# Kernel tuning notes

Measured on AMD Instinct MI355X. Metric: run time of the kernel, lower is better.

Reference implementation:

```python
import jax, jax.numpy as jnp
import numpy as np
import math

B, NB, NA, NC, D, E, H = 4, 2048, 1024, 1024, 1024, 8, 16
HD = D // H
TOP_K = 2
T_MAX = 1000.0
TAU_MIN, TAU_MAX = 0.5, 2.0
W_MIN, W_MAX = 0.1, 0.2
CAP_LO, CAP_HI = 0.5, 0.6
FLOOR = min(0.05, 0.15 / E)       # cfg.routing_floor property
ALPHA = min(FLOOR * E, 1.0)       # routing-floor interpolation weight
BIAS_COEFF = 0.01
EPS = 1e-8


def _layernorm(x, g, b, eps=1e-5):
    mu = x.mean(-1, keepdims=True)
    var = ((x - mu) ** 2).mean(-1, keepdims=True)
    return (x - mu) * jax.lax.rsqrt(var + eps) * g + b


def _forward(tokens_B, output_A, output_C, in_proj_w, in_proj_b, out_proj_w, out_proj_b,
             ln_g, ln_b, te_w1, te_b1, te_w2, te_b2,
             gate_w1, gate_b1, gate_w2, gate_b2, expert_bias, t):
    t_norm = t.astype(jnp.float32) / T_MAX                 # (B,)
    ctx_C = jax.lax.stop_gradient(output_C)                # stopgrad_C_to_B
    ctx_AC = jnp.concatenate([output_A, ctx_C], axis=1)    # (B, NA+NC, D)

    # --- cross attention (torch nn.MultiheadAttention, batch_first) ---
    wq, wk, wv = jnp.split(in_proj_w, 3, axis=0)
    bq, bk, bv = jnp.split(in_proj_b, 3)
    q = (tokens_B @ wq.T + bq).reshape(B, NB, H, HD)
    k = (ctx_AC @ wk.T + bk).reshape(B, NA + NC, H, HD)
    v = (ctx_AC @ wv.T + bv).reshape(B, NA + NC, H, HD)
    scores = jnp.einsum('bqhd,bkhd->bhqk', q, k) / math.sqrt(HD)
    attn = jax.nn.softmax(scores, axis=-1)
    ctx = jnp.einsum('bhqk,bkhd->bqhd', attn, v).reshape(B, NB, D)
    ctx_B = ctx @ out_proj_w.T + out_proj_b
    ctx_B = _layernorm(ctx_B + tokens_B, ln_g, ln_b)

    # --- sinusoidal timestep embedding + 2-layer MLP ---
    half = D // 2
    freq = jnp.exp(-math.log(10000.0) * jnp.arange(half, dtype=jnp.float32) / (half - 1))
    args = t.astype(jnp.float32)[:, None] * freq
    emb = jnp.concatenate([jnp.sin(args), jnp.cos(args)], axis=-1)   # (B, D)
    t_emb = jax.nn.silu(emb @ te_w1.T + te_b1) @ te_w2.T + te_b2     # (B, D)
    t_emb = jnp.broadcast_to(t_emb[:, None, :], (B, NB, D))

    # --- gate MLP + expert bias + temperature ---
    gate_in = jnp.concatenate([tokens_B, ctx_B, t_emb], axis=-1)     # (B, NB, 3D)
    logits = jax.nn.relu(gate_in @ gate_w1.T + gate_b1) @ gate_w2.T + gate_b2 + expert_bias
    tau = (TAU_MIN + (TAU_MAX - TAU_MIN) * t_norm)[:, None, None]
    probs = jax.nn.softmax(logits / tau, axis=-1)                    # (B, NB, E)

    # routing floor: interpolate toward uniform
    probs = (1.0 - ALPHA) * probs + ALPHA / E

    # shared expert injection: expert 0 gets scheduled weight w(t), rest renormalised
    w = (W_MIN + (W_MAX - W_MIN) * t_norm)[:, None, None]
    shared = jnp.maximum(probs[..., 0:1], w)
    others = probs[..., 1:]
    others = others / jnp.maximum(others.sum(-1, keepdims=True), EPS) * (1.0 - shared)
    probs = jnp.concatenate([shared, others], axis=-1)

    # top-k mask (keep top-k probs, zero the rest)
    vals, idx = jax.lax.top_k(probs, TOP_K)
    dispatch = (jax.nn.one_hot(idx, E, dtype=probs.dtype) * vals[..., None]).sum(-2)

    # token-level hard cap (torch.no_grad -> stop_gradient) with redistribution
    cap = (CAP_LO + (CAP_HI - CAP_LO) * t_norm)[:, None, None]
    excess = jax.nn.relu(dispatch - cap)
    capped = dispatch - excess
    headroom = jax.nn.relu(cap - capped)
    head_sum = jnp.maximum(headroom.sum(-1, keepdims=True), EPS)
    capped = capped + excess.sum(-1, keepdims=True) * (headroom / head_sum)
    dispatch = jax.lax.stop_gradient(capped)

    # batch-level utilisation penalty on specialists 1..E-1
    fair = NB / max(E - 1, 1)
    load = dispatch.sum(axis=1).mean(axis=0)                          # (E,)
    pen_excess = jax.nn.relu(load[1:] - fair * 1.5)
    bias_penalty = BIAS_COEFF * jnp.sum(pen_excess ** 2)

    combine = dispatch / (dispatch.sum(-1, keepdims=True) + EPS)
    return dispatch, combine, bias_penalty


def setup_inputs() -> dict:
    key = jax.random.key(0)
    ks = jax.random.split(key, 12)
    g = lambda k, sh: jax.random.normal(k, sh, jnp.float32) * 0.02
    return dict(
        tokens_B=jax.random.normal(ks[0], (B, NB, D), jnp.float32),
        output_A=jax.random.normal(ks[1], (B, NA, D), jnp.float32),
        output_C=jax.random.normal(ks[2], (B, NC, D), jnp.float32),
        t=jax.random.randint(ks[3], (B,), 0, 1000, jnp.int32),
        in_proj_w=g(ks[4], (3 * D, D)),
        in_proj_b=jnp.zeros((3 * D,), jnp.float32),
        out_proj_w=g(ks[5], (D, D)),
        out_proj_b=jnp.zeros((D,), jnp.float32),
        ln_g=jnp.ones((D,), jnp.float32),
        ln_b=jnp.zeros((D,), jnp.float32),
        te_w1=g(ks[6], (2 * D, D)),
        te_b1=jnp.zeros((2 * D,), jnp.float32),
        te_w2=g(ks[7], (D, 2 * D)),
        te_b2=jnp.zeros((D,), jnp.float32),
        gate_w1=g(ks[8], (D, 3 * D)),
        gate_b1=jnp.zeros((D,), jnp.float32),
        gate_w2=g(ks[9], (E, D)),
        gate_b2=jnp.zeros((E,), jnp.float32),
        expert_bias=jnp.zeros((E,), jnp.float32),
    )


def reference(tokens_B, output_A, output_C, t, in_proj_w, in_proj_b, out_proj_w, out_proj_b,
              ln_g, ln_b, te_w1, te_b1, te_w2, te_b2,
              gate_w1, gate_b1, gate_w2, gate_b2, expert_bias):
    return _forward(tokens_B, output_A, output_C, in_proj_w, in_proj_b, out_proj_w, out_proj_b,
                    ln_g, ln_b, te_w1, te_b1, te_w2, te_b2,
                    gate_w1, gate_b1, gate_w2, gate_b2, expert_bias, t)
```

## Files before the change

kernel.cpp:

```cpp
#include <hip/hip_runtime.h>
#include <math.h>


typedef __attribute__((ext_vector_type(8))) short short8;
typedef __attribute__((ext_vector_type(4))) short sh4;
typedef __attribute__((ext_vector_type(4))) float f32x4;
typedef __attribute__((ext_vector_type(4))) unsigned int u32x4;
typedef unsigned short u16;
typedef unsigned int u32;

__global__ void zero_k(double* p) {
    if (threadIdx.x < 8) p[threadIdx.x] = 0.0;
}

__device__ inline u16 bf_hi(float x) {
    u32 u = __float_as_uint(x);
    u += 0x7FFFu + ((u >> 16) & 1u);
    return (u16)(u >> 16);
}
__device__ inline u16 bf_lo(float x, u16 h) {
    float hf = __uint_as_float(((u32)h) << 16);
    return bf_hi(x - hf);
}
__device__ inline u32 pack_bf(float x) {
    u32 u = __float_as_uint(x);
    u32 hi = (u + (0x7FFFu + ((u >> 16) & 1u))) >> 16;
    float hf = __uint_as_float(hi << 16);
    float d = x - hf;
    u32 u2 = __float_as_uint(d);
    u32 lo = (u2 + (0x7FFFu + ((u2 >> 16) & 1u))) >> 16;
    return (hi << 16) | lo;
}

__device__ inline void pack2(float p0, float p1, u32& o0, u32& o1) {
    u32 h01, l01;
    asm("v_cvt_pk_bf16_f32 %0, %1, %2" : "=v"(h01) : "v"(p0), "v"(p1));
    float d0 = p0 - __uint_as_float(h01 << 16);
    float d1 = p1 - __uint_as_float(h01 & 0xffff0000u);
    asm("v_cvt_pk_bf16_f32 %0, %1, %2" : "=v"(l01) : "v"(d0), "v"(d1));
    o0 = __builtin_amdgcn_perm(h01, l01, 0x05040100u);
    o1 = __builtin_amdgcn_perm(h01, l01, 0x07060302u);
}

__device__ inline void pfrag(const f32x4 s, sh4& hi, sh4& lo, float& acc) {
    float p0 = exp2f(s[0]), p1 = exp2f(s[1]), p2 = exp2f(s[2]), p3 = exp2f(s[3]);
    acc += (p0 + p1) + (p2 + p3);
    u32 h01, h23, l01, l23;
    asm("v_cvt_pk_bf16_f32 %0, %1, %2" : "=v"(h01) : "v"(p0), "v"(p1));
    asm("v_cvt_pk_bf16_f32 %0, %1, %2" : "=v"(h23) : "v"(p2), "v"(p3));
    float d0 = p0 - __uint_as_float(h01 << 16);
    float d1 = p1 - __uint_as_float(h01 & 0xffff0000u);
    float d2 = p2 - __uint_as_float(h23 << 16);
    float d3 = p3 - __uint_as_float(h23 & 0xffff0000u);
    asm("v_cvt_pk_bf16_f32 %0, %1, %2" : "=v"(l01) : "v"(d0), "v"(d1));
    asm("v_cvt_pk_bf16_f32 %0, %1, %2" : "=v"(l23) : "v"(d2), "v"(d3));
    union { u32 u[2]; sh4 s4; } H, L;
    H.u[0] = h01; H.u[1] = h23;
    L.u[0] = l01; L.u[1] = l23;
    hi = H.s4; lo = L.s4;
}

__device__ inline f32x4 mfma32(short8 a, short8 b, f32x4 c) {
    return __builtin_amdgcn_mfma_f32_16x16x32_bf16(a, b, c, 0, 0, 0);
}
__device__ inline f32x4 mfma16(sh4 a, sh4 b, f32x4 c) {
#if __has_builtin(__builtin_amdgcn_mfma_f32_16x16x16bf16_1k)
    return __builtin_amdgcn_mfma_f32_16x16x16bf16_1k(a, b, c, 0, 0, 0);
#else
    asm volatile("v_mfma_f32_16x16x16_bf16 %0, %1, %2, %0"
                 : "+v"(c) : "v"(a), "v"(b));
    return c;
#endif
}

__device__ inline void async16(const u16* g, u16* l) {
    __builtin_amdgcn_global_load_lds(
        (const __attribute__((address_space(1))) unsigned int*)g,
        (__attribute__((address_space(3))) unsigned int*)l,
        16, 0, 0);
}

__global__ __launch_bounds__(256)
void split_k(const float* __restrict__ in, u16* __restrict__ hi,
             u16* __restrict__ lo, int n4) {
    int i = blockIdx.x * 256 + threadIdx.x;
    if (i >= n4) return;
    float4 x = ((const float4*)in)[i];
    ushort4 h, l;
    h.x = bf_hi(x.x); l.x = bf_lo(x.x, h.x);
    h.y = bf_hi(x.y); l.y = bf_lo(x.y, h.y);
    h.z = bf_hi(x.z); l.z = bf_lo(x.z, h.z);
    h.w = bf_hi(x.w); l.w = bf_lo(x.w, h.w);
    ((ushort4*)hi)[i] = h;
    ((ushort4*)lo)[i] = l;
}

__global__ void emb_k(const int* __restrict__ t, float* __restrict__ emb) {
    int b = blockIdx.x;
    int j = threadIdx.x;
    float x1 = (float)(-9.210340371976184) * (float)j;
    float x2 = x1 / 511.0f;
    float freq = (float)exp((double)x2);
    float tf = (float)t[b];
    float arg = tf * freq;
    emb[b * 1024 + j]       = (float)sin((double)arg);
    emb[b * 1024 + 512 + j] = (float)cos((double)arg);
}

__global__ void te_fc_k(const float* __restrict__ in, const float* __restrict__ W,
                        const float* __restrict__ bias, float* __restrict__ out,
                        int K, int N, int do_silu) {
    int b = blockIdx.x;
    int wv = threadIdx.x >> 6, lane = threadIdx.x & 63;
    const float* inb = in + (size_t)b * K;
    int n0 = blockIdx.y * 16 + wv * 4;
    for (int q = 0; q < 4; q++) {
        int n = n0 + q;
        const float* wr = W + (size_t)n * K;
        float acc = 0.f;
        for (int c = lane * 4; c < K; c += 256) {
            float4 a  = *(const float4*)(inb + c);
            float4 w4 = *(const float4*)(wr + c);
            acc += a.x * w4.x + a.y * w4.y + a.z * w4.z + a.w * w4.w;
        }
#pragma unroll
        for (int off = 1; off < 64; off <<= 1) acc += __shfl_xor(acc, off, 64);
        if (lane == 0) {
            float x = acc + bias[n];
            out[(size_t)b * N + n] = do_silu ? (x / (1.0f + expf(-x))) : x;
        }
    }
}

template<bool GATE, bool RELU, int OMODE>
__global__ __launch_bounds__(256, 2)
void bfgemm_k(const u16* __restrict__ A0h, const u16* __restrict__ A0l,
              const u16* __restrict__ A1h, const u16* __restrict__ A1l,
              const u16* __restrict__ A2h, const u16* __restrict__ A2l,
              const u16* __restrict__ Wh_g, const u16* __restrict__ Wl_g,
              const float* __restrict__ bias, float* __restrict__ C,
              u16* __restrict__ Chi, u16* __restrict__ Clo, int K, float scale)
{
    __shared__ u16 Ah[128 * 32];
    __shared__ u16 Al[128 * 32];
    __shared__ u16 Wh[128 * 32];
    __shared__ u16 Wl[128 * 32];
    const int tid = threadIdx.x;
    const int row0 = blockIdx.x * 128;
    const int col0 = blockIdx.y * 128;
    const int wv = tid >> 6;
    const int lane = tid & 63;
    const int wrow = (wv & 1) * 64;
    const int wcol = (wv >> 1) * 64;
    const int l15 = lane & 15, quad = lane >> 4;

    f32x4 acc[4][4];
#pragma unroll
    for (int i = 0; i < 4; i++)
#pragma unroll
        for (int j = 0; j < 4; j++)
            acc[i][j] = (f32x4){0.f, 0.f, 0.f, 0.f};

    const int ar0 = tid >> 2, ak0 = (tid & 3) * 8;
    const int ar1 = (tid + 256) >> 2, ak1 = ((tid + 256) & 3) * 8;

    for (int kc = 0; kc < K; kc += 32) {
        const u16* pAh = A0h;
        const u16* pAl = A0l;
        int kk = kc;
        int tembseg = 0;
        if (GATE) {
            int seg = kc >> 10;
            if (seg == 1) { pAh = A1h; pAl = A1l; }
            else if (seg == 2) { pAh = A2h; pAl = A2l; tembseg = 1; }
            kk = kc & 1023;
        }
        const int astr = GATE ? 1024 : K;
        int g0 = row0 + ar0, g1 = row0 + ar1;
        if (GATE && tembseg) { g0 >>= 11; g1 >>= 11; }
        uint4 vah0 = *(const uint4*)&pAh[(size_t)g0 * astr + kk + ak0];
        uint4 vah1 = *(const uint4*)&pAh[(size_t)g1 * astr + kk + ak1];
        uint4 val0 = *(const uint4*)&pAl[(size_t)g0 * astr + kk + ak0];
        uint4 val1 = *(const uint4*)&pAl[(size_t)g1 * astr + kk + ak1];
        uint4 vwh0 = *(const uint4*)&Wh_g[(size_t)(col0 + ar0) * K + kc + ak0];
        uint4 vwh1 = *(const uint4*)&Wh_g[(size_t)(col0 + ar1) * K + kc + ak1];
        uint4 vwl0 = *(const uint4*)&Wl_g[(size_t)(col0 + ar0) * K + kc + ak0];
        uint4 vwl1 = *(const uint4*)&Wl_g[(size_t)(col0 + ar1) * K + kc + ak1];
        __syncthreads();
        *(uint4*)&Ah[ar0 * 32 + ak0] = vah0;
        *(uint4*)&Ah[ar1 * 32 + ak1] = vah1;
        *(uint4*)&Al[ar0 * 32 + ak0] = val0;
        *(uint4*)&Al[ar1 * 32 + ak1] = val1;
        *(uint4*)&Wh[ar0 * 32 + ak0] = vwh0;
        *(uint4*)&Wh[ar1 * 32 + ak1] = vwh1;
        *(uint4*)&Wl[ar0 * 32 + ak0] = vwl0;
        *(uint4*)&Wl[ar1 * 32 + ak1] = vwl1;
        __syncthreads();

        short8 a_h[4], a_l[4];
#pragma unroll
        for (int i = 0; i < 4; i++) {
            int r = (wrow + i * 16 + l15) * 32 + quad * 8;
            a_h[i] = *(const short8*)&Ah[r];
            a_l[i] = *(const short8*)&Al[r];
        }
#pragma unroll
        for (int j = 0; j < 4; j++) {
            int c = (wcol + j * 16 + l15) * 32 + quad * 8;
            short8 b_h = *(const short8*)&Wh[c];
            short8 b_l = *(const short8*)&Wl[c];
#pragma unroll
            for (int i = 0; i < 4; i++) {
                acc[i][j] = __builtin_amdgcn_mfma_f32_16x16x32_bf16(a_h[i], b_h, acc[i][j], 0, 0, 0);
                acc[i][j] = __builtin_amdgcn_mfma_f32_16x16x32_bf16(a_h[i], b_l, acc[i][j], 0, 0, 0);
                acc[i][j] = __builtin_amdgcn_mfma_f32_16x16x32_bf16(a_l[i], b_h, acc[i][j], 0, 0, 0);
            }
        }
    }

#pragma unroll
    for (int i = 0; i < 4; i++) {
#pragma unroll
        for (int j = 0; j < 4; j++) {
            int cc = col0 + wcol + j * 16 + l15;
#pragma unroll
            for (int r = 0; r < 4; r++) {
                int rr = row0 + wrow + i * 16 + quad * 4 + r;
                float v = (acc[i][j][r] + ((OMODE == 3) ? bias[rr] : bias[cc])) * scale;
                if (RELU) v = fmaxf(v, 0.f);
                if (OMODE == 0) {
                    C[(size_t)rr * 1024 + cc] = v;
                } else if (OMODE == 1) {
                    u32 pk = pack_bf(v);
                    size_t a = (size_t)rr * 1024 + cc;
                    Chi[a] = (u16)(pk >> 16); Clo[a] = (u16)pk;
                } else if (OMODE == 2) {
                    int orow = ((rr >> 10) & 3) * 2048 + (rr >> 12) * 1024 + (rr & 1023);
                    u32 pk = pack_bf(v);
                    size_t a = (size_t)orow * 1024 + cc;
                    Chi[a] = (u16)(pk >> 16); Clo[a] = (u16)pk;
                } else {
                    int bb2 = (cc >> 10) & 3;
                    int key = (cc >> 12) * 1024 + (cc & 1023);
                    u32 pk = pack_bf(v);
                    size_t a = ((size_t)(bb2 * 1024 + rr)) * 2048 + key;
                    Chi[a] = (u16)(pk >> 16); Clo[a] = (u16)pk;
                }
            }
        }
    }
}

__global__ __launch_bounds__(512, 4)
void attn_k(const u16* Qh, const u16* Ql,
            const u16* __restrict__ Kh, const u16* __restrict__ Kl,
            const u16* __restrict__ Vh, const u16* __restrict__ Vl,
            u16* Oh, u16* Ol)
{
    __shared__ __align__(16) u16 smem[32768];
    u16* Kbase = smem;
    u16* Vbase = smem + 16384;

    const int tid = threadIdx.x;
    const int w = tid >> 6, lane = tid & 63;
    const int l15 = lane & 15, quad = lane >> 4;
    const int bh = blockIdx.x, b = bh >> 4, h = bh & 15;
    const int qw = blockIdx.y * 256 + w * 32;
    const int qrow0 = b * 2048 + qw;

    short8 qh_f[2][2], ql_f[2][2];
#pragma unroll
    for (int i = 0; i < 2; i++)
#pragma unroll
        for (int kc = 0; kc < 2; kc++) {
            size_t a = (size_t)(qrow0 + i * 16 + l15) * 1024 + h * 64 + kc * 32 + quad * 8;
            qh_f[i][kc] = *(const short8*)&Qh[a];
            ql_f[i][kc] = *(const short8*)&Ql[a];
        }

    const int srow = tid >> 3;
    const int scsw = ((tid & 7) ^ (srow & 7)) << 3;
    const size_t gk_base = ((size_t)(b * 2048) + srow) * 1024 + h * 64 + scsw;
    const size_t gv_base = ((size_t)((b * 16 + h) * 64 + srow)) * 2048 + scsw;

    f32x4 o[4][2];
#pragma unroll
    for (int dt = 0; dt < 4; dt++)
#pragma unroll
        for (int i = 0; i < 2; i++) o[dt][i] = (f32x4){0.f, 0.f, 0.f, 0.f};
    float lsum[2] = {0.f, 0.f};

    {
        u16* kd = Kbase + w * 512;
        u16* vd = Vbase + w * 512;
        async16(&Kh[gk_base], kd);
        async16(&Kl[gk_base], kd + 4096);
        async16(&Vh[gv_base], vd);
        async16(&Vl[gv_base], vd + 4096);
    }
    __syncthreads();

    for (int kt = 0; kt < 32; kt++) {
        const int cur = kt & 1;
        if (kt < 31) {
            const int nxt = cur ^ 1;
            const size_t gk = gk_base + (size_t)(kt + 1) * 65536;
            const size_t gv = gv_base + (size_t)(kt + 1) * 64;
            u16* kd = Kbase + nxt * 8192 + w * 512;
            u16* vd = Vbase + nxt * 8192 + w * 512;
            async16(&Kh[gk], kd);
            async16(&Kl[gk], kd + 4096);
            async16(&Vh[gv], vd);
            async16(&Vl[gv], vd + 4096);
        }
        const u16* Ksh = Kbase + cur * 8192;
        const u16* Ksl = Ksh + 4096;
        const u16* Vsh = Vbase + cur * 8192;
        const u16* Vsl = Vsh + 4096;

#pragma unroll
        for (int jt = 0; jt < 4; jt++) {
            f32x4 st0 = (f32x4){0.f, 0.f, 0.f, 0.f};
            f32x4 st1 = (f32x4){0.f, 0.f, 0.f, 0.f};
            const int ka = (jt * 16 + l15) * 64 + ((quad ^ (l15 & 7)) << 3);
            short8 kh0 = *(const short8*)&Ksh[ka];
            short8 kh1 = *(const short8*)&Ksh[ka ^ 32];
            short8 kl0 = *(const short8*)&Ksl[ka];
            short8 kl1 = *(const short8*)&Ksl[ka ^ 32];
            st0 = mfma32(kh0, qh_f[0][0], st0);
            st0 = mfma32(kl0, qh_f[0][0], st0);
            st0 = mfma32(kh0, ql_f[0][0], st0);
            st0 = mfma32(kh1, qh_f[0][1], st0);
            st0 = mfma32(kl1, qh_f[0][1], st0);
            st0 = mfma32(kh1, ql_f[0][1], st0);
            st1 = mfma32(kh0, qh_f[1][0], st1);
            st1 = mfma32(kl0, qh_f[1][0], st1);
            st1 = mfma32(kh0, ql_f[1][0], st1);
            st1 = mfma32(kh1, qh_f[1][1], st1);
            st1 = mfma32(kl1, qh_f[1][1], st1);
            st1 = mfma32(kh1, ql_f[1][1], st1);
            sh4 phi0, plo0, phi1, plo1;
            pfrag(st0, phi0, plo0, lsum[0]);
            pfrag(st1, phi1, plo1, lsum[1]);
#pragma unroll
            for (int dt = 0; dt < 4; dt++) {
                const int va = (dt * 16 + l15) * 64
                             + (((jt * 2 + (quad >> 1)) ^ (l15 & 7)) << 3)
                             + (quad & 1) * 4;
                sh4 vvh = *(const sh4*)&Vsh[va];
                sh4 vvl = *(const sh4*)&Vsl[va];
                o[dt][0] = mfma16(vvh, phi0, o[dt][0]);
                o[dt][0] = mfma16(vvl, phi0, o[dt][0]);
                o[dt][0] = mfma16(vvh, plo0, o[dt][0]);
                o[dt][1] = mfma16(vvh, phi1, o[dt][1]);
                o[dt][1] = mfma16(vvl, phi1, o[dt][1]);
                o[dt][1] = mfma16(vvh, plo1, o[dt][1]);
            }
        }
        __syncthreads();
    }

#pragma unroll
    for (int i = 0; i < 2; i++) {
        float s2 = lsum[i];
        s2 += __shfl_xor(s2, 16, 64);
        s2 += __shfl_xor(s2, 32, 64);
        lsum[i] = 1.0f / s2;
    }

    u32* otr = (u32*)smem + w * 2048;
#pragma unroll
    for (int i = 0; i < 2; i++) {
        const int q = i * 16 + l15;
        const int xm = (q & 7) << 2;
#pragma unroll
        for (int dt = 0; dt < 4; dt++) {
#pragma unroll
            for (int r = 0; r < 4; r += 2) {
                float v0 = o[dt][i][r]     * lsum[i];
                float v1 = o[dt][i][r + 1] * lsum[i];
                u32 a0, a1;
                pack2(v0, v1, a0, a1);
                const int d = dt * 16 + quad * 4 + r;
                uint2 val; val.x = a0; val.y = a1;
                *(uint2*)&otr[q * 64 + (d ^ xm)] = val;
            }
        }
    }
    const int qr = lane >> 1;
    const int dh = lane & 1;
    const size_t gq = (size_t)(qrow0 + qr) * 1024 + h * 64 + dh * 32;
#pragma unroll
    for (int g = 0; g < 4; g++) {
        const int c0 = dh * 8 + g * 2;
        const int m = qr & 7;
        uint4 x = *(const uint4*)&otr[qr * 64 + ((c0 ^ m) << 2)];
        uint4 y = *(const uint4*)&otr[qr * 64 + (((c0 + 1) ^ m) << 2)];
        union { short8 s; u32x4 u; } hh, ll;
        hh.u = (u32x4){ __builtin_amdgcn_perm(x.y, x.x, 0x07060302u),
                        __builtin_amdgcn_perm(x.w, x.z, 0x07060302u),
                        __builtin_amdgcn_perm(y.y, y.x, 0x07060302u),
                        __builtin_amdgcn_perm(y.w, y.z, 0x07060302u) };
        ll.u = (u32x4){ __builtin_amdgcn_perm(x.y, x.x, 0x05040100u),
                        __builtin_amdgcn_perm(x.w, x.z, 0x05040100u),
                        __builtin_amdgcn_perm(y.y, y.x, 0x05040100u),
                        __builtin_amdgcn_perm(y.w, y.z, 0x05040100u) };
        *(short8*)&Oh[gq + g * 8] = hh.s;
        *(short8*)&Ol[gq + g * 8] = ll.s;
    }
}

__global__ __launch_bounds__(256)
void ln_split_k(const float* __restrict__ X, const float* __restrict__ T,
                const float* __restrict__ g, const float* __restrict__ bta,
                u16* __restrict__ chi, u16* __restrict__ clo)
{
    __shared__ float red[8];
    int r = blockIdx.x, tid = threadIdx.x;
    size_t base = (size_t)r * 1024 + tid * 4;
    float4 x  = *(const float4*)(X + base);
    float4 tk = *(const float4*)(T + base);
    x.x += tk.x; x.y += tk.y; x.z += tk.z; x.w += tk.w;
    float s = x.x + x.y + x.z + x.w;
#pragma unroll
    for (int off = 1; off < 64; off <<= 1) s += __shfl_xor(s, off, 64);
    int wv = tid >> 6;
    if ((tid & 63) == 0) red[wv] = s;
    __syncthreads();
    float mu = (red[0] + red[1] + red[2] + red[3]) * (1.0f / 1024.0f);
    float dx0 = x.x - mu, dx1 = x.y - mu, dx2 = x.z - mu, dx3 = x.w - mu;
    float ss = dx0 * dx0 + dx1 * dx1 + dx2 * dx2 + dx3 * dx3;
#pragma unroll
    for (int off = 1; off < 64; off <<= 1) ss += __shfl_xor(ss, off, 64);
    if ((tid & 63) == 0) red[4 + wv] = ss;
    __syncthreads();
    float var = (red[4] + red[5] + red[6] + red[7]) * (1.0f / 1024.0f);
    float inv = 1.0f / sqrtf(var + 1e-5f);
    float4 gg = *(const float4*)(g + tid * 4);
    float4 bb = *(const float4*)(bta + tid * 4);
    float y0 = dx0 * inv * gg.x + bb.x;
    float y1 = dx1 * inv * gg.y + bb.y;
    float y2 = dx2 * inv * gg.z + bb.z;
    float y3 = dx3 * inv * gg.w + bb.w;
    ushort4 h, l;
    h.x = bf_hi(y0); l.x = bf_lo(y0, h.x);
    h.y = bf_hi(y1); l.y = bf_lo(y1, h.y);
    h.z = bf_hi(y2); l.z = bf_lo(y2, h.z);
    h.w = bf_hi(y3); l.w = bf_lo(y3, h.w);
    *(ushort4*)&chi[base] = h;
    *(ushort4*)&clo[base] = l;
}

__global__ __launch_bounds__(256)
void logits_k(const float* __restrict__ Hd, const float* __restrict__ W2,
              const float* __restrict__ b2, const float* __restrict__ eb,
              float* __restrict__ Lg)
{
    int gw = (blockIdx.x * 256 + threadIdx.x) >> 6;
    int lane = threadIdx.x & 63;
    const float* h = Hd + (size_t)gw * 1024;
    float4 hv[4];
#pragma unroll
    for (int j = 0; j < 4; j++) hv[j] = *(const float4*)(h + j * 256 + lane * 4);
    float res[8];
#pragma unroll
    for (int e = 0; e < 8; e++) {
        const float* w = W2 + (size_t)e * 1024;
        float acc = 0.f;
#pragma unroll
        for (int j = 0; j < 4; j++) {
            float4 w4 = *(const float4*)(w + j * 256 + lane * 4);
            acc += hv[j].x * w4.x + hv[j].y * w4.y + hv[j].z * w4.z + hv[j].w * w4.w;
        }
#pragma unroll
        for (int off = 1; off < 64; off <<= 1) acc += __shfl_xor(acc, off, 64);
        res[e] = acc;
    }
    if (lane < 8) {
        float v = res[0];
#pragma unroll
        for (int e = 1; e < 8; e++) v = (lane == e) ? res[e] : v;
        Lg[(size_t)gw * 8 + lane] = v + b2[lane] + eb[lane];
    }
}

__global__ __launch_bounds__(256)
void router_k(const float* __restrict__ Lg, const int* __restrict__ t,
              float* __restrict__ outp, double* __restrict__ loadAcc)
{
    __shared__ double wred[4][8];
    int tid = threadIdx.x;
    int r = blockIdx.x * 256 + tid;
    int b = r >> 11;
    float tn  = (float)t[b] / 1000.0f;
    float tau = 0.5f + 1.5f * tn;
    float p[8];
    float mx = -INFINITY;
#pragma unroll
    for (int e = 0; e < 8; e++) { p[e] = Lg[(size_t)r * 8 + e] / tau; mx = fmaxf(mx, p[e]); }
    float sum = 0.f;
#pragma unroll
    for (int e = 0; e < 8; e++) { p[e] = expf(p[e] - mx); sum += p[e]; }
#pragma unroll
    for (int e = 0; e < 8; e++) p[e] = p[e] / sum;
#pragma unroll
    for (int e = 0; e < 8; e++) p[e] = 0.85f * p[e] + 0.01875f;
    float w = 0.1f + 0.1f * tn;
    float shared_p = fmaxf(p[0], w);
    float osum = 0.f;
#pragma unroll
    for (int e = 1; e < 8; e++) osum += p[e];
    float denom_o = fmaxf(osum, 1e-8f);
    float one_m = 1.0f - shared_p;
    p[0] = shared_p;
#pragma unroll
    for (int e = 1; e < 8; e++) p[e] = (p[e] / denom_o) * one_m;
    int i0 = 0; float v0 = p[0];
#pragma unroll
    for (int e = 1; e < 8; e++) if (p[e] > v0) { v0 = p[e]; i0 = e; }
    int i1 = -1; float v1 = -INFINITY;
#pragma unroll
    for (int e = 0; e < 8; e++) if (e != i0 && p[e] > v1) { v1 = p[e]; i1 = e; }
    float cap = 0.5f + 0.1f * tn;
    float dsp[8], capped[8], hr[8];
    float exsum = 0.f, hsum = 0.f;
#pragma unroll
    for (int e = 0; e < 8; e++) {
        float d = ((e == i0) ? v0 : 0.f) + ((e == i1) ? v1 : 0.f);
        float ex = fmaxf(d - cap, 0.f);
        float c = d - ex;
        float hh = fmaxf(cap - c, 0.f);
        capped[e] = c; hr[e] = hh;
        exsum += ex; hsum += hh;
    }
    float hden = fmaxf(hsum, 1e-8f);
    float dsum = 0.f;
#pragma unroll
    for (int e = 0; e < 8; e++) {
        float d = capped[e] + exsum * (hr[e] / hden);
        dsp[e] = d; dsum += d;
    }
    float cden = dsum + 1e-8f;
#pragma unroll
    for (int e = 0; e < 8; e++) {
        outp[(size_t)r * 8 + e] = dsp[e];
        outp[65536 + (size_t)r * 8 + e] = dsp[e] / cden;
    }
    int lane = tid & 63, wv = tid >> 6;
#pragma unroll
    for (int e = 0; e < 8; e++) {
        double s = (double)dsp[e];
#pragma unroll
        for (int off = 1; off < 64; off <<= 1) s += __shfl_xor(s, off, 64);
        if (lane == 0) wred[wv][e] = s;
    }
    __syncthreads();
    if (tid < 8) {
        double s = wred[0][tid] + wred[1][tid] + wred[2][tid] + wred[3][tid];
        atomicAdd(&loadAcc[tid], s);
    }
}

__global__ void penalty_k(const double* __restrict__ loadAcc, float* __restrict__ outp) {
    if (threadIdx.x == 0) {
        const float thr = (float)(2048.0 / 7.0 * 1.5);
        float pen = 0.f;
#pragma unroll
        for (int e = 1; e < 8; e++) {
            float load = (float)(loadAcc[e] / 4.0);
            float x = fmaxf(load - thr, 0.f);
            pen += x * x;
        }
        outp[131072] = 0.01f * pen;
    }
}

extern "C" void kernel_launch(void* const* d_in, const int* in_sizes, int n_in,
                              void* d_out, int out_size, void* d_ws, size_t ws_size,
                              hipStream_t stream)
{
    const float* tokens = (const float*)d_in[0];
    const float* outA   = (const float*)d_in[1];
    const float* outC   = (const float*)d_in[2];
    const int*   tt     = (const int*)  d_in[3];
    const float* in_w   = (const float*)d_in[4];
    const float* in_b   = (const float*)d_in[5];
    const float* op_w   = (const float*)d_in[6];
    const float* op_b   = (const float*)d_in[7];
    const float* lng    = (const float*)d_in[8];
    const float* lnb    = (const float*)d_in[9];
    const float* te_w1  = (const float*)d_in[10];
    const float* te_b1  = (const float*)d_in[11];
    const float* te_w2  = (const float*)d_in[12];
    const float* te_b2  = (const float*)d_in[13];
    const float* g_w1   = (const float*)d_in[14];
    const float* g_b1   = (const float*)d_in[15];
    const float* g_w2   = (const float*)d_in[16];
    const float* g_b2   = (const float*)d_in[17];
    const float* e_bias = (const float*)d_in[18];
    float* out = (float*)d_out;

    float* ws = (float*)d_ws;
    const size_t NM = (size_t)8192 * 1024;
    float* F0     = ws;
    float* temb   = ws + NM;
    float* embb   = temb + 4096;
    float* hte    = embb + 4096;
    float* logitsb = hte + 8192;
    double* loads = (double*)(logitsb + 65536);

    u16* U = (u16*)(loads + 16);
    u16* Tokh = U;
    u16* Tokl = Tokh + NM;
    u16* ActH = Tokl + NM;
    u16* ActL = ActH + NM;
    u16* Qh   = ActL + NM;
    u16* Ql   = Qh + NM;
    u16* Kh   = Ql + NM;
    u16* Kl   = Kh + NM;
    u16* Vth  = Kl + NM;
    u16* Vtl  = Vth + NM;
    u16* Wsh  = Vtl + NM;
    u16* Wsl  = Wsh + (size_t)3 * 1024 * 1024;
    u16* Tbh  = Wsl + (size_t)3 * 1024 * 1024;
    u16* Tbl  = Tbh + 4096;

    zero_k<<<1, 64, 0, stream>>>(loads);
    emb_k<<<4, 512, 0, stream>>>(tt, embb);
    te_fc_k<<<dim3(4, 128), 256, 0, stream>>>(embb, te_w1, te_b1, hte, 1024, 2048, 1);
    te_fc_k<<<dim3(4, 64),  256, 0, stream>>>(hte,  te_w2, te_b2, temb, 2048, 1024, 0);

    split_k<<<8192, 256, 0, stream>>>(tokens, Tokh, Tokl, 8192 * 1024 / 4);
    split_k<<<3072, 256, 0, stream>>>(in_w, Wsh, Wsl, 3 * 1024 * 1024 / 4);
    split_k<<<4096, 256, 0, stream>>>(outA, ActH, ActL, 4096 * 1024 / 4);
    split_k<<<4096, 256, 0, stream>>>(outC, ActH + (size_t)4096 * 1024,
                                      ActL + (size_t)4096 * 1024, 4096 * 1024 / 4);

    bfgemm_k<false, false, 1><<<dim3(64, 8), 256, 0, stream>>>(
        Tokh, Tokl, nullptr, nullptr, nullptr, nullptr,
        Wsh, Wsl, in_b, nullptr, Qh, Ql, 1024, 0.18033688011112042f);
    bfgemm_k<false, false, 2><<<dim3(64, 8), 256, 0, stream>>>(
        ActH, ActL, nullptr, nullptr, nullptr, nullptr,
        Wsh + (size_t)1024 * 1024, Wsl + (size_t)1024 * 1024,
        in_b + 1024, nullptr, Kh, Kl, 1024, 1.0f);
    bfgemm_k<false, false, 3><<<dim3(8, 64), 256, 0, stream>>>(
        Wsh + (size_t)2048 * 1024, Wsl + (size_t)2048 * 1024,
        nullptr, nullptr, nullptr, nullptr,
        ActH, ActL, in_b + 2048, nullptr, Vth, Vtl, 1024, 1.0f);

    attn_k<<<dim3(64, 8), 512, 0, stream>>>(Qh, Ql, Kh, Kl, Vth, Vtl, Qh, Ql);

    split_k<<<1024, 256, 0, stream>>>(op_w, Wsh, Wsl, 1024 * 1024 / 4);
    bfgemm_k<false, false, 0><<<dim3(64, 8), 256, 0, stream>>>(
        Qh, Ql, nullptr, nullptr, nullptr, nullptr,
        Wsh, Wsl, op_b, F0, nullptr, nullptr, 1024, 1.0f);

    ln_split_k<<<8192, 256, 0, stream>>>(F0, tokens, lng, lnb, Kh, Kl);

    split_k<<<4, 256, 0, stream>>>(temb, Tbh, Tbl, 4096 / 4);
    split_k<<<3072, 256, 0, stream>>>(g_w1, Wsh, Wsl, 3072 * 1024 / 4);
    bfgemm_k<true, true, 0><<<dim3(64, 8), 256, 0, stream>>>(
        Tokh, Tokl, Kh, Kl, Tbh, Tbl,
        Wsh, Wsl, g_b1, F0, nullptr, nullptr, 3072, 1.0f);

    logits_k<<<2048, 256, 0, stream>>>(F0, g_w2, g_b2, e_bias, logitsb);
    router_k<<<32, 256, 0, stream>>>(logitsb, tt, out, loads);
    penalty_k<<<1, 64, 0, stream>>>(loads, out);
}
```

Before: 834.1 us.

## Double-buffer bf16x3 GEMM tiles in LDS with async global-to-LDS loads

Replaces the register-staged load/store of A and W hi/lo tiles with async 16-byte global-to-LDS copies into a two-stage shared-memory buffer. The next K-chunk is issued before computing on the current one, so only one barrier per iteration remains and memory latency can overlap the MFMA work. LDS use doubles to 64 KB per block, which may limit the occupancy targeted by launch_bounds(256,2). Correctness relies on async16 being waited on before the barrier.

```diff
diff --git a/kernel.cpp b/kernel.cpp
--- a/kernel.cpp
+++ b/kernel.cpp
@@ -141,10 +141,7 @@
               const float* __restrict__ bias, float* __restrict__ C,
               u16* __restrict__ Chi, u16* __restrict__ Clo, int K, float scale)
 {
-    __shared__ u16 Ah[128 * 32];
-    __shared__ u16 Al[128 * 32];
-    __shared__ u16 Wh[128 * 32];
-    __shared__ u16 Wl[128 * 32];
+    __shared__ __align__(16) u16 smem[2][4][4096];
     const int tid = threadIdx.x;
     const int row0 = blockIdx.x * 128;
     const int col0 = blockIdx.y * 128;
@@ -161,54 +158,55 @@
         for (int j = 0; j < 4; j++)
             acc[i][j] = (f32x4){0.f, 0.f, 0.f, 0.f};
 
-    const int ar0 = tid >> 2, ak0 = (tid & 3) * 8;
-    const int ar1 = (tid + 256) >> 2, ak1 = ((tid + 256) & 3) * 8;
+    const int ar0 = tid >> 2, akc = (tid & 3) * 8;
+    const int woff = wv * 512;
+
+#define BF_STAGE(KC, BUF) do {                                                 \
+        const u16* pAh_ = A0h; const u16* pAl_ = A0l;                          \
+        int kk_ = (KC); int ts_ = 0;                                           \
+        if (GATE) {                                                            \
+            int sg_ = (KC) >> 10;                                              \
+            if (sg_ == 1) { pAh_ = A1h; pAl_ = A1l; }                          \
+            else if (sg_ == 2) { pAh_ = A2h; pAl_ = A2l; ts_ = 1; }            \
+            kk_ = (KC) & 1023;                                                 \
+        }                                                                      \
+        const int astr_ = GATE ? 1024 : K;                                     \
+        int g0_ = row0 + ar0, g1_ = row0 + ar0 + 64;                           \
+        if (GATE && ts_) { g0_ >>= 11; g1_ >>= 11; }                           \
+        u16* b_ = &smem[BUF][0][0] + woff;                                     \
+        async16(&pAh_[(size_t)g0_ * astr_ + kk_ + akc], b_);                   \
+        async16(&pAh_[(size_t)g1_ * astr_ + kk_ + akc], b_ + 2048);            \
+        async16(&pAl_[(size_t)g0_ * astr_ + kk_ + akc], b_ + 4096);            \
+        async16(&pAl_[(size_t)g1_ * astr_ + kk_ + akc], b_ + 6144);            \
+        async16(&Wh_g[(size_t)(col0 + ar0) * K + (KC) + akc], b_ + 8192);      \
+        async16(&Wh_g[(size_t)(col0 + ar0 + 64) * K + (KC) + akc], b_ + 10240);\
+        async16(&Wl_g[(size_t)(col0 + ar0) * K + (KC) + akc], b_ + 12288);     \
+        async16(&Wl_g[(size_t)(col0 + ar0 + 64) * K + (KC) + akc], b_ + 14336);\
+    } while (0)
+
+    BF_STAGE(0, 0);
+    __syncthreads();
 
     for (int kc = 0; kc < K; kc += 32) {
-        const u16* pAh = A0h;
-        const u16* pAl = A0l;
-        int kk = kc;
-        int tembseg = 0;
-        if (GATE) {
-            int seg = kc >> 10;
-            if (seg == 1) { pAh = A1h; pAl = A1l; }
-            else if (seg == 2) { pAh = A2h; pAl = A2l; tembseg = 1; }
-            kk = kc & 1023;
-        }
-        const int astr = GATE ? 1024 : K;
-        int g0 = row0 + ar0, g1 = row0 + ar1;
-        if (GATE && tembseg) { g0 >>= 11; g1 >>= 11; }
-        uint4 vah0 = *(const uint4*)&pAh[(size_t)g0 * astr + kk + ak0];
-        uint4 vah1 = *(const uint4*)&pAh[(size_t)g1 * astr + kk + ak1];
-        uint4 val0 = *(const uint4*)&pAl[(size_t)g0 * astr + kk + ak0];
-        uint4 val1 = *(const uint4*)&pAl[(size_t)g1 * astr + kk + ak1];
-        uint4 vwh0 = *(const uint4*)&Wh_g[(size_t)(col0 + ar0) * K + kc + ak0];
-        uint4 vwh1 = *(const uint4*)&Wh_g[(size_t)(col0 + ar1) * K + kc + ak1];
-        uint4 vwl0 = *(const uint4*)&Wl_g[(size_t)(col0 + ar0) * K + kc + ak0];
-        uint4 vwl1 = *(const uint4*)&Wl_g[(size_t)(col0 + ar1) * K + kc + ak1];
-        __syncthreads();
-        *(uint4*)&Ah[ar0 * 32 + ak0] = vah0;
-        *(uint4*)&Ah[ar1 * 32 + ak1] = vah1;
-        *(uint4*)&Al[ar0 * 32 + ak0] = val0;
-        *(uint4*)&Al[ar1 * 32 + ak1] = val1;
-        *(uint4*)&Wh[ar0 * 32 + ak0] = vwh0;
-        *(uint4*)&Wh[ar1 * 32 + ak1] = vwh1;
-        *(uint4*)&Wl[ar0 * 32 + ak0] = vwl0;
-        *(uint4*)&Wl[ar1 * 32 + ak1] = vwl1;
-        __syncthreads();
+        const int cur = (kc >> 5) & 1;
+        if (kc + 32 < K) BF_STAGE(kc + 32, cur ^ 1);
+        const u16* Ahs = smem[cur][0];
+        const u16* Als = smem[cur][1];
+        const u16* Whs = smem[cur][2];
+        const u16* Wls = smem[cur][3];
 
         short8 a_h[4], a_l[4];
 #pragma unroll
         for (int i = 0; i < 4; i++) {
             int r = (wrow + i * 16 + l15) * 32 + quad * 8;
-            a_h[i] = *(const short8*)&Ah[r];
-            a_l[i] = *(const short8*)&Al[r];
+            a_h[i] = *(const short8*)&Ahs[r];
+            a_l[i] = *(const short8*)&Als[r];
         }
 #pragma unroll
         for (int j = 0; j < 4; j++) {
             int c = (wcol + j * 16 + l15) * 32 + quad * 8;
-            short8 b_h = *(const short8*)&Wh[c];
-            short8 b_l = *(const short8*)&Wl[c];
+            short8 b_h = *(const short8*)&Whs[c];
+            short8 b_l = *(const short8*)&Wls[c];
 #pragma unroll
             for (int i = 0; i < 4; i++) {
                 acc[i][j] = __builtin_amdgcn_mfma_f32_16x16x32_bf16(a_h[i], b_h, acc[i][j], 0, 0, 0);
@@ -216,7 +214,9 @@
                 acc[i][j] = __builtin_amdgcn_mfma_f32_16x16x32_bf16(a_l[i], b_h, acc[i][j], 0, 0, 0);
             }
         }
-    }
+        __syncthreads();
+    }
+#undef BF_STAGE
 
 #pragma unroll
     for (int i = 0; i < 4; i++) {
```

New measurement: 862.7 us. 1.03x slower.
